# Kernel optimization log

Hardware: AMD Instinct MI355X
Metric: run time of the kernel (lower is better)

Reference implementation:

```python
import jax, jax.numpy as jnp
import numpy as np

N = 100_000      # nodes
E = 1_600_000    # directed edges (avg degree 16)
F_IN = 128       # num_node_features
H = 8            # heads in conv1
C = 32           # hidden_channels
G = 64           # graphs in batch
NC = 10          # num_classes


def setup_inputs() -> dict:
    key = jax.random.key(0)
    ks = jax.random.split(key, 12)
    gl = lambda k, shape, fan: (jax.random.normal(k, shape, jnp.float32) / np.sqrt(fan)).astype(jnp.float32)
    return {
        "x": jax.random.normal(ks[0], (N, F_IN), jnp.float32),
        "edge_index": jax.random.randint(ks[1], (2, E), 0, N, dtype=jnp.int32),
        "batch": jnp.sort(jax.random.randint(ks[2], (N,), 0, G, dtype=jnp.int32)),
        "W1": gl(ks[3], (F_IN, H * C), F_IN),
        "att_src1": gl(ks[4], (H, C), C),
        "att_dst1": gl(ks[5], (H, C), C),
        "b1": jnp.zeros((H * C,), jnp.float32),
        "W2": gl(ks[6], (H * C, C), H * C),
        "att_src2": gl(ks[7], (1, C), C),
        "att_dst2": gl(ks[8], (1, C), C),
        "b2": jnp.zeros((C,), jnp.float32),
        "Wlin": gl(ks[9], (C, NC), C),
        "blin": jnp.zeros((NC,), jnp.float32),
    }


def gat_conv(x, src, dst, W, att_src, att_dst, bias, heads, ch, concat):
    """PyG GATConv (eval mode): gather, LeakyReLU(0.2) scores, segment softmax over dst, scatter-sum."""
    n = x.shape[0]
    h = (x @ W).reshape(n, heads, ch)                     # [N,H,C]
    a_s = jnp.sum(h * att_src, axis=-1)                   # [N,H]
    a_d = jnp.sum(h * att_dst, axis=-1)                   # [N,H]
    e = jax.nn.leaky_relu(a_s[src] + a_d[dst], 0.2)       # [E,H]
    m = jax.ops.segment_max(e, dst, num_segments=n)       # [N,H], stable softmax
    p = jnp.exp(e - m[dst])
    z = jax.ops.segment_sum(p, dst, num_segments=n)
    coef = p / (z[dst] + 1e-16)                           # [E,H]
    out = jax.ops.segment_sum(coef[:, :, None] * h[src], dst, num_segments=n)  # [N,H,C]
    out = out.reshape(n, heads * ch) if concat else out.mean(axis=1)
    return out + bias


def reference(x, edge_index, batch, W1, att_src1, att_dst1, b1,
              W2, att_src2, att_dst2, b2, Wlin, blin):
    n = x.shape[0]
    loops = jnp.arange(n, dtype=edge_index.dtype)         # GATConv add_self_loops=True
    src = jnp.concatenate([edge_index[0], loops])
    dst = jnp.concatenate([edge_index[1], loops])

    h = gat_conv(x, src, dst, W1, att_src1, att_dst1, b1, H, C, concat=True)
    h = jax.nn.elu(h)                                     # dropout is identity in eval
    h = gat_conv(h, src, dst, W2, att_src2, att_dst2, b2, 1, C, concat=False)

    # global_mean_pool over graph ids
    sums = jax.ops.segment_sum(h, batch, num_segments=G)  # [G,C]
    cnts = jax.ops.segment_sum(jnp.ones((n,), h.dtype), batch, num_segments=G)
    pooled = sums / jnp.maximum(cnts, 1.0)[:, None]

    return pooled @ Wlin + blin                           # [G,NC]
```

## Files before the change

### kernel.cpp

```cpp
#include <hip/hip_runtime.h>
#include <cstdint>

#define NN 100000
#define EE 1600000
#define GG 64
#define FIN 128
#define HC 256
#define NC 10

typedef short v8s __attribute__((ext_vector_type(8)));
typedef float v4f __attribute__((ext_vector_type(4)));

static __device__ __forceinline__ float lrelu(float x) { return x > 0.f ? x : 0.2f * x; }
static __device__ __forceinline__ float bf2f(unsigned short b) {
  return __uint_as_float(((unsigned int)b) << 16);
}
static __device__ __forceinline__ unsigned short f2bf(float f) {
  unsigned int u = __float_as_uint(f);
  unsigned int r = (u + 0x7FFFu + ((u >> 16) & 1u)) >> 16;
  return (unsigned short)r;
}
static __device__ __forceinline__ void unpack2(unsigned int u, float& f0, float& f1) {
  f0 = __uint_as_float(u << 16);
  f1 = __uint_as_float(u & 0xFFFF0000u);
}

__global__ __launch_bounds__(256) void k_prepx(const float* __restrict__ x,
                                               unsigned short* __restrict__ xb,
                                               const int* __restrict__ ei,
                                               int* __restrict__ counts) {
  const int idx = blockIdx.x * 256 + threadIdx.x;
  const int i4 = idx * 4;
  float4 v = *(const float4*)(x + i4);
  ushort4 u;
  u.x = f2bf(v.x); u.y = f2bf(v.y); u.z = f2bf(v.z); u.w = f2bf(v.w);
  *(ushort4*)(xb + i4) = u;
  if (idx < EE) atomicAdd(&counts[ei[EE + idx]], 1);
}

__global__ void k_prep(const float* __restrict__ W1, unsigned short* __restrict__ W1tg) {
  const int b = blockIdx.x, t = threadIdx.x;
  if (t < 128) W1tg[b * 128 + t] = f2bf(W1[t * HC + b]);
}

__global__ void k_prepw2(const float* __restrict__ W2,
                         unsigned short* __restrict__ W2thi,
                         unsigned short* __restrict__ W2tlo) {
  const int b = blockIdx.x;
  const int t = threadIdx.x;
  float w = W2[t * 32 + b];
  unsigned short hi = f2bf(w);
  W2thi[b * 256 + t] = hi;
  W2tlo[b * 256 + t] = f2bf(w - bf2f(hi));
}

__global__ __launch_bounds__(256) void k_gemm1(const unsigned short* __restrict__ xb,
                                               const unsigned short* __restrict__ W1tg,
                                               const float* __restrict__ att_src1,
                                               const float* __restrict__ att_dst1,
                                               unsigned short* __restrict__ h1b,
                                               float* __restrict__ as1,
                                               float* __restrict__ ad1) {
  const int t = threadIdx.x;
  const int m0 = blockIdx.x * 64;
  const int n0 = blockIdx.y * 128;
  const int hb = blockIdx.y * 4;
  const int lane = t & 63;
  const int wm = t >> 6;
  const int ml = lane & 15;
  const int quad = lane >> 4;
  int row = m0 + wm * 16 + ml; if (row >= NN) row = NN - 1;
  v4f acc[8];
#pragma unroll
  for (int tt = 0; tt < 8; ++tt) acc[tt] = (v4f){0.f, 0.f, 0.f, 0.f};
#pragma unroll
  for (int kk = 0; kk < 4; ++kk) {
    const int k0 = kk * 32 + quad * 8;
    v8s a = *(const v8s*)(xb + (size_t)row * FIN + k0);
#pragma unroll
    for (int tt = 0; tt < 8; ++tt) {
      v8s b = *(const v8s*)(W1tg + (size_t)(n0 + tt * 16 + ml) * FIN + k0);
      acc[tt] = __builtin_amdgcn_mfma_f32_16x16x32_bf16(a, b, acc[tt], 0, 0, 0);
    }
  }
#pragma unroll
  for (int tt = 0; tt < 8; ++tt) {
#pragma unroll
    for (int r = 0; r < 4; ++r) {
      int rg = m0 + wm * 16 + quad * 4 + r;
      if (rg < NN) h1b[(size_t)rg * HC + n0 + tt * 16 + ml] = f2bf(acc[tt][r]);
    }
  }
  float ps[4][4], pd[4][4];
#pragma unroll
  for (int i = 0; i < 4; ++i)
#pragma unroll
    for (int r = 0; r < 4; ++r) { ps[i][r] = 0.f; pd[i][r] = 0.f; }
#pragma unroll
  for (int i = 0; i < 4; ++i) {
#pragma unroll
    for (int half = 0; half < 2; ++half) {
      const int tt = 2 * i + half;
      const float a_s = att_src1[(hb + i) * 32 + half * 16 + ml];
      const float a_d = att_dst1[(hb + i) * 32 + half * 16 + ml];
#pragma unroll
      for (int r = 0; r < 4; ++r) {
        ps[i][r] += acc[tt][r] * a_s;
        pd[i][r] += acc[tt][r] * a_d;
      }
    }
  }
#pragma unroll
  for (int i = 0; i < 4; ++i) {
#pragma unroll
    for (int r = 0; r < 4; ++r) {
      float s = ps[i][r], d = pd[i][r];
      s += __shfl_xor(s, 1, 64); s += __shfl_xor(s, 2, 64);
      s += __shfl_xor(s, 4, 64); s += __shfl_xor(s, 8, 64);
      d += __shfl_xor(d, 1, 64); d += __shfl_xor(d, 2, 64);
      d += __shfl_xor(d, 4, 64); d += __shfl_xor(d, 8, 64);
      ps[i][r] = s; pd[i][r] = d;
    }
  }
  if (ml == 0) {
#pragma unroll
    for (int r = 0; r < 4; ++r) {
      int rg = m0 + wm * 16 + quad * 4 + r;
      if (rg < NN) {
#pragma unroll
        for (int i = 0; i < 4; ++i) {
          as1[rg * 8 + hb + i] = ps[i][r];
          ad1[rg * 8 + hb + i] = pd[i][r];
        }
      }
    }
  }
}

__global__ void k_scan1(const int* __restrict__ counts, int* __restrict__ offs,
                        int* __restrict__ bsums) {
  __shared__ int s[256];
  const int t = threadIdx.x;
  const int i = blockIdx.x * 256 + t;
  int v = (i < NN) ? counts[i] : 0;
  s[t] = v;
  __syncthreads();
  for (int off = 1; off < 256; off <<= 1) {
    int tv = (t >= off) ? s[t - off] : 0;
    __syncthreads();
    s[t] += tv;
    __syncthreads();
  }
  if (i < NN) offs[i] = s[t] - v;
  if (t == 255) bsums[blockIdx.x] = s[255];
}

__global__ void k_scan2(int* __restrict__ bsums, int nb) {
  __shared__ int s[512];
  const int t = threadIdx.x;
  int v = (t < nb) ? bsums[t] : 0;
  s[t] = v;
  __syncthreads();
  for (int off = 1; off < 512; off <<= 1) {
    int tv = (t >= off) ? s[t - off] : 0;
    __syncthreads();
    s[t] += tv;
    __syncthreads();
  }
  if (t < nb) bsums[t] = s[t] - v;
}

__global__ void k_scan3(int* __restrict__ offs, const int* __restrict__ bsums,
                        int* __restrict__ cursor) {
  const int i = blockIdx.x * 256 + threadIdx.x;
  if (i < NN) {
    int v = offs[i] + bsums[i >> 8];
    offs[i] = v;
    cursor[i] = v;
  }
  if (i == 0) offs[NN] = EE;
}

__global__ void k_scatter(const int* __restrict__ ei, int* __restrict__ cursor,
                          int* __restrict__ esrc) {
  int e = blockIdx.x * 256 + threadIdx.x;
  if (e < EE) {
    int s = ei[e];
    int d = ei[EE + e];
    int p = atomicAdd(&cursor[d], 1);
    esrc[p] = s;
  }
}

__global__ __launch_bounds__(256) void k_agg1(const unsigned short* __restrict__ h1b,
                                              const float* __restrict__ as1,
                                              const float* __restrict__ ad1,
                                              const int* __restrict__ offs,
                                              const int* __restrict__ esrc,
                                              const float* __restrict__ b1,
                                              const unsigned short* __restrict__ W2thi,
                                              const unsigned short* __restrict__ W2tlo,
                                              const float* __restrict__ att_src2,
                                              const float* __restrict__ att_dst2,
                                              unsigned short* __restrict__ h2b,
                                              float* __restrict__ as2,
                                              float* __restrict__ ad2) {
  __shared__ float wl[4][8][36];
  __shared__ __attribute__((aligned(16))) unsigned short o1hi[4][272];
  __shared__ __attribute__((aligned(16))) unsigned short o1lo[4][272];
  const int t = threadIdx.x;
  const int lane = t & 63;
  const int w = t >> 6;
  const int n0 = blockIdx.x * 4;
  const int nu = __builtin_amdgcn_readfirstlane(n0 + w);
  const int head = lane >> 3;
  const uint2* __restrict__ h1u2 = (const uint2*)h1b;
  const int start = offs[nu], end = offs[nu + 1];
  const float4 dnA = *(const float4*)(ad1 + (size_t)nu * 8);
  const float4 dnB = *(const float4*)(ad1 + (size_t)nu * 8 + 4);
  const float4 dn4 = (lane & 32) ? dnB : dnA;

  float z, a0, a1, a2, a3;
  {
    float w0 = __expf(lrelu(as1[nu * 8 + head] + ad1[nu * 8 + head]));
    uint2 q = h1u2[(size_t)nu * 64 + lane];
    float f0, f1, f2, f3; unpack2(q.x, f0, f1); unpack2(q.y, f2, f3);
    z = w0; a0 = w0 * f0; a1 = w0 * f1; a2 = w0 * f2; a3 = w0 * f3;
  }
  for (int base = start; base < end; base += 32) {
    const int cnt = min(32, end - base);
    const int l5 = lane & 31;
    int s = 0;
    if (l5 < cnt) s = esrc[base + l5];
    const int hb4 = (lane >> 5) << 2;
    const float4 av = *(const float4*)(as1 + (size_t)s * 8 + hb4);
    float w0 = __expf(lrelu(av.x + dn4.x));
    float w1 = __expf(lrelu(av.y + dn4.y));
    float w2 = __expf(lrelu(av.z + dn4.z));
    float w3 = __expf(lrelu(av.w + dn4.w));
    const bool act = l5 < cnt;
    wl[w][hb4 + 0][l5] = act ? w0 : 0.f;
    wl[w][hb4 + 1][l5] = act ? w1 : 0.f;
    wl[w][hb4 + 2][l5] = act ? w2 : 0.f;
    wl[w][hb4 + 3][l5] = act ? w3 : 0.f;
    const int cnt4 = (cnt + 3) & ~3;
    int jb = 0;
    for (; jb + 8 <= cnt4; jb += 8) {
      uint2 q[8];
#pragma unroll
      for (int u = 0; u < 8; ++u) {
        const int sj = esrc[base + jb + u];
        q[u] = h1u2[(size_t)sj * 64 + lane];
      }
      const float4 wq0 = *(const float4*)&wl[w][head][jb];
      const float4 wq1 = *(const float4*)&wl[w][head][jb + 4];
      z += ((wq0.x + wq0.y) + (wq0.z + wq0.w)) + ((wq1.x + wq1.y) + (wq1.z + wq1.w));
      float f0, f1, f2, f3;
      unpack2(q[0].x, f0, f1); unpack2(q[0].y, f2, f3);
      a0 += wq0.x * f0; a1 += wq0.x * f1; a2 += wq0.x * f2; a3 += wq0.x * f3;
      unpack2(q[1].x, f0, f1); unpack2(q[1].y, f2, f3);
      a0 += wq0.y * f0; a1 += wq0.y * f1; a2 += wq0.y * f2; a3 += wq0.y * f3;
      unpack2(q[2].x, f0, f1); unpack2(q[2].y, f2, f3);
      a0 += wq0.z * f0; a1 += wq0.z * f1; a2 += wq0.z * f2; a3 += wq0.z * f3;
      unpack2(q[3].x, f0, f1); unpack2(q[3].y, f2, f3);
      a0 += wq0.w * f0; a1 += wq0.w * f1; a2 += wq0.w * f2; a3 += wq0.w * f3;
      unpack2(q[4].x, f0, f1); unpack2(q[4].y, f2, f3);
      a0 += wq1.x * f0; a1 += wq1.x * f1; a2 += wq1.x * f2; a3 += wq1.x * f3;
      unpack2(q[5].x, f0, f1); unpack2(q[5].y, f2, f3);
      a0 += wq1.y * f0; a1 += wq1.y * f1; a2 += wq1.y * f2; a3 += wq1.y * f3;
      unpack2(q[6].x, f0, f1); unpack2(q[6].y, f2, f3);
      a0 += wq1.z * f0; a1 += wq1.z * f1; a2 += wq1.z * f2; a3 += wq1.z * f3;
      unpack2(q[7].x, f0, f1); unpack2(q[7].y, f2, f3);
      a0 += wq1.w * f0; a1 += wq1.w * f1; a2 += wq1.w * f2; a3 += wq1.w * f3;
    }
    if (jb < cnt4) {
      uint2 q[4];
#pragma unroll
      for (int u = 0; u < 4; ++u) {
        const int sj = esrc[base + jb + u];
        q[u] = h1u2[(size_t)sj * 64 + lane];
      }
      const float4 wq0 = *(const float4*)&wl[w][head][jb];
      z += (wq0.x + wq0.y) + (wq0.z + wq0.w);
      float f0, f1, f2, f3;
      unpack2(q[0].x, f0, f1); unpack2(q[0].y, f2, f3);
      a0 += wq0.x * f0; a1 += wq0.x * f1; a2 += wq0.x * f2; a3 += wq0.x * f3;
      unpack2(q[1].x, f0, f1); unpack2(q[1].y, f2, f3);
      a0 += wq0.y * f0; a1 += wq0.y * f1; a2 += wq0.y * f2; a3 += wq0.y * f3;
      unpack2(q[2].x, f0, f1); unpack2(q[2].y, f2, f3);
      a0 += wq0.z * f0; a1 += wq0.z * f1; a2 += wq0.z * f2; a3 += wq0.z * f3;
      unpack2(q[3].x, f0, f1); unpack2(q[3].y, f2, f3);
      a0 += wq0.w * f0; a1 += wq0.w * f1; a2 += wq0.w * f2; a3 += wq0.w * f3;
    }
  }
  {
    const float zi = 1.0f / (z + 1e-16f);
    const float4 bb = *(const float4*)(b1 + 4 * lane);
    float v0 = a0 * zi + bb.x;
    float v1 = a1 * zi + bb.y;
    float v2 = a2 * zi + bb.z;
    float v3 = a3 * zi + bb.w;
    v0 = v0 > 0.f ? v0 : (__expf(v0) - 1.0f);
    v1 = v1 > 0.f ? v1 : (__expf(v1) - 1.0f);
    v2 = v2 > 0.f ? v2 : (__expf(v2) - 1.0f);
    v3 = v3 > 0.f ? v3 : (__expf(v3) - 1.0f);
    ushort4 hh, ll;
    hh.x = f2bf(v0); hh.y = f2bf(v1); hh.z = f2bf(v2); hh.w = f2bf(v3);
    ll.x = f2bf(v0 - bf2f(hh.x));
    ll.y = f2bf(v1 - bf2f(hh.y));
    ll.z = f2bf(v2 - bf2f(hh.z));
    ll.w = f2bf(v3 - bf2f(hh.w));
    *(ushort4*)&o1hi[w][4 * lane] = hh;
    *(ushort4*)&o1lo[w][4 * lane] = ll;
  }
  __syncthreads();
  if (w == 0) {
    const int ml = lane & 15;
    const int quad = lane >> 4;
    const int mr = ml & 3;
    v4f acc[2];
    acc[0] = (v4f){0.f, 0.f, 0.f, 0.f};
    acc[1] = (v4f){0.f, 0.f, 0.f, 0.f};
#pragma unroll
    for (int kk = 0; kk < 8; ++kk) {
      const int k0 = kk * 32 + quad * 8;
      v8s ah = *(const v8s*)&o1hi[mr][k0];
      v8s al = *(const v8s*)&o1lo[mr][k0];
#pragma unroll
      for (int tt = 0; tt < 2; ++tt) {
        v8s bh = *(const v8s*)(W2thi + (size_t)(tt * 16 + ml) * 256 + k0);
        v8s bl = *(const v8s*)(W2tlo + (size_t)(tt * 16 + ml) * 256 + k0);
        acc[tt] = __builtin_amdgcn_mfma_f32_16x16x32_bf16(ah, bh, acc[tt], 0, 0, 0);
        acc[tt] = __builtin_amdgcn_mfma_f32_16x16x32_bf16(al, bh, acc[tt], 0, 0, 0);
        acc[tt] = __builtin_amdgcn_mfma_f32_16x16x32_bf16(ah, bl, acc[tt], 0, 0, 0);
      }
    }
    if (quad == 0) {
      const float s0 = att_src2[ml], s1 = att_src2[16 + ml];
      const float d0 = att_dst2[ml], d1 = att_dst2[16 + ml];
#pragma unroll
      for (int r = 0; r < 4; ++r) {
        const int nn = n0 + r;
        const float h0 = acc[0][r], h1v = acc[1][r];
        h2b[(size_t)nn * 32 + ml] = f2bf(h0);
        h2b[(size_t)nn * 32 + 16 + ml] = f2bf(h1v);
        float ps = h0 * s0 + h1v * s1;
        float pd = h0 * d0 + h1v * d1;
        ps += __shfl_xor(ps, 1, 64); ps += __shfl_xor(ps, 2, 64);
        ps += __shfl_xor(ps, 4, 64); ps += __shfl_xor(ps, 8, 64);
        pd += __shfl_xor(pd, 1, 64); pd += __shfl_xor(pd, 2, 64);
        pd += __shfl_xor(pd, 4, 64); pd += __shfl_xor(pd, 8, 64);
        if (ml == 0) { as2[nn] = ps; ad2[nn] = pd; }
      }
    }
  }
}

__global__ __launch_bounds__(256) void k_agg2(const unsigned short* __restrict__ h2b,
                                              const float* __restrict__ as2,
                                              const float* __restrict__ ad2,
                                              const int* __restrict__ offs,
                                              const int* __restrict__ esrc,
                                              const float* __restrict__ b2,
                                              float* __restrict__ h3) {
  __shared__ int2 swl[4][64];
  const int t = threadIdx.x;
  const int lane = t & 63;
  const int wv = t >> 6;
  const int n = __builtin_amdgcn_readfirstlane(blockIdx.x * 4 + wv);
  const int col = lane & 15;
  const int slot = lane >> 4;
  const unsigned int* __restrict__ h2u = (const unsigned int*)h2b;
  const int start = offs[n], end = offs[n + 1];
  const float adn = ad2[n];
  float z = 0.f, acc0 = 0.f, acc1 = 0.f;
  if (slot == 0) {
    float w0 = __expf(lrelu(as2[n] + adn));
    unsigned int q = h2u[(unsigned)(n * 16 + col)];
    float f0, f1; unpack2(q, f0, f1);
    z = w0; acc0 = w0 * f0; acc1 = w0 * f1;
  }
  for (int base = start; base < end; base += 64) {
    const int cnt = min(64, end - base);
    int s = 0; float wgt = 0.f;
    if (lane < cnt) {
      s = esrc[base + lane];
      wgt = __expf(lrelu(as2[s] + adn));
    }
    swl[wv][lane] = make_int2(s, __float_as_int(wgt));
    const int nit = (cnt + 7) >> 3;
#pragma unroll 2
    for (int j = 0; j < nit; ++j) {
      const int2 p0 = swl[wv][8 * j + slot];
      const int2 p1 = swl[wv][8 * j + 4 + slot];
      const unsigned int q0 = h2u[(unsigned)(p0.x * 16 + col)];
      const unsigned int q1 = h2u[(unsigned)(p1.x * 16 + col)];
      const float wj0 = __int_as_float(p0.y);
      const float wj1 = __int_as_float(p1.y);
      float f0, f1, g0, g1;
      unpack2(q0, f0, f1); unpack2(q1, g0, g1);
      z += wj0 + wj1;
      acc0 += wj0 * f0; acc0 += wj1 * g0;
      acc1 += wj0 * f1; acc1 += wj1 * g1;
    }
  }
  acc0 += __shfl_xor(acc0, 16, 64); acc0 += __shfl_xor(acc0, 32, 64);
  acc1 += __shfl_xor(acc1, 16, 64); acc1 += __shfl_xor(acc1, 32, 64);
  z    += __shfl_xor(z, 16, 64);    z    += __shfl_xor(z, 32, 64);
  if (slot == 0) {
    const float zi = 1.0f / (z + 1e-16f);
    float2 bb = *(const float2*)(b2 + 2 * col);
    float2 o;
    o.x = acc0 * zi + bb.x;
    o.y = acc1 * zi + bb.y;
    *(float2*)(h3 + (size_t)n * 32 + 2 * col) = o;
  }
}

__global__ __launch_bounds__(256) void k_poolfin(const float* __restrict__ h3,
                                                 const int* __restrict__ batch,
                                                 const float* __restrict__ Wlin,
                                                 const float* __restrict__ blin,
                                                 float* __restrict__ out) {
  __shared__ int bounds[2];
  __shared__ float red[8][33];
  __shared__ float mean[32];
  const int g = blockIdx.x;
  const int t = threadIdx.x;
  if (t < 2) {
    int target = g + t;
    int lo = 0, hi = NN;
    while (lo < hi) { int mid = (lo + hi) >> 1; if (batch[mid] < target) lo = mid + 1; else hi = mid; }
    bounds[t] = lo;
  }
  __syncthreads();
  const int lo = bounds[0], hi = bounds[1];
  const int rr = t >> 5, c = t & 31;
  float a = 0.f;
  for (int r = lo + rr; r < hi; r += 8) a += h3[(size_t)r * 32 + c];
  red[rr][c] = a;
  __syncthreads();
  if (rr == 0) {
    float s = 0.f;
#pragma unroll
    for (int i = 0; i < 8; ++i) s += red[i][c];
    float ct = (float)(hi - lo);
    ct = ct > 1.f ? ct : 1.f;
    mean[c] = s / ct;
  }
  __syncthreads();
  if (t < NC) {
    float acc = 0.f;
#pragma unroll
    for (int cc = 0; cc < 32; ++cc) acc += mean[cc] * Wlin[cc * NC + t];
    out[g * NC + t] = acc + blin[t];
  }
}

extern "C" void kernel_launch(void* const* d_in, const int* in_sizes, int n_in,
                              void* d_out, int out_size, void* d_ws, size_t ws_size,
                              hipStream_t stream) {
  const float* x        = (const float*)d_in[0];
  const int*   ei       = (const int*)d_in[1];
  const int*   batch    = (const int*)d_in[2];
  const float* W1       = (const float*)d_in[3];
  const float* att_src1 = (const float*)d_in[4];
  const float* att_dst1 = (const float*)d_in[5];
  const float* b1       = (const float*)d_in[6];
  const float* W2       = (const float*)d_in[7];
  const float* att_src2 = (const float*)d_in[8];
  const float* att_dst2 = (const float*)d_in[9];
  const float* b2       = (const float*)d_in[10];
  const float* Wlin     = (const float*)d_in[11];
  const float* blin     = (const float*)d_in[12];
  float* out = (float*)d_out;
  char* ws = (char*)d_ws;

  unsigned short* h1b   = (unsigned short*)(ws + 0);
  unsigned short* xb    = (unsigned short*)(ws + 51200000);
  float* h3     = (float*)(ws + 51200000);
  float* as1    = (float*)(ws + 76800000);
  float* ad1    = (float*)(ws + 80000000);
  int* counts   = (int*)(ws + 83200000);
  int* offs     = (int*)(ws + 83600000);
  int* cursor   = (int*)(ws + 84000256);
  int* esrc     = (int*)(ws + 84400256);
  int* bsums    = (int*)(ws + 90800320);
  unsigned short* h2b   = (unsigned short*)(ws + 90801920);
  float* as2    = (float*)(ws + 97201920);
  float* ad2    = (float*)(ws + 97601920);
  unsigned short* W1tg  = (unsigned short*)(ws + 98001920);
  unsigned short* W2thi = (unsigned short*)(ws + 98067456);
  unsigned short* W2tlo = (unsigned short*)(ws + 98083840);

  const int nb_scan = (NN + 255) / 256;

  hipMemsetAsync(counts, 0, NN * sizeof(int), stream);
  hipMemsetAsync(ws + 90800256, 0, 64, stream);
  k_prepx<<<12500, 256, 0, stream>>>(x, xb, ei, counts);
  k_prep<<<256, 128, 0, stream>>>(W1, W1tg);
  k_prepw2<<<32, 256, 0, stream>>>(W2, W2thi, W2tlo);

  dim3 g1((NN + 63) / 64, 2);
  k_gemm1<<<g1, 256, 0, stream>>>(xb, W1tg, att_src1, att_dst1, h1b, as1, ad1);

  k_scan1<<<nb_scan, 256, 0, stream>>>(counts, offs, bsums);
  k_scan2<<<1, 512, 0, stream>>>(bsums, nb_scan);
  k_scan3<<<nb_scan, 256, 0, stream>>>(offs, bsums, cursor);
  k_scatter<<<(EE + 255) / 256, 256, 0, stream>>>(ei, cursor, esrc);

  k_agg1<<<NN / 4, 256, 0, stream>>>(h1b, as1, ad1, offs, esrc, b1, W2thi, W2tlo,
                                     att_src2, att_dst2, h2b, as2, ad2);

  k_agg2<<<NN / 4, 256, 0, stream>>>(h2b, as2, ad2, offs, esrc, b2, h3);
  k_poolfin<<<GG, 256, 0, stream>>>(h3, batch, Wlin, blin, out);
}
```

Measured before the change: 622.4 us.

## Widen gathers in GAT aggregation kernels and merge prep kernels into one launch

The layer-1 aggregation now has each half-wave gather a full 512-byte h1 row with 16-byte loads, so two edges are processed in parallel per wave, and the halves are combined with a cross-half shuffle. Layer-2 aggregation likewise uses 8-byte loads with 8 edges per pass, reduced by a three-step shuffle. The three preprocessing kernels are merged into one launch to cut launch overhead. The aim is fewer, wider memory transactions per gathered row, at the cost of more registers per thread and extra shuffle reductions.

```diff
diff --git a/kernel.cpp b/kernel.cpp
--- a/kernel.cpp
+++ b/kernel.cpp
@@ -10,6 +10,7 @@
 
 typedef short v8s __attribute__((ext_vector_type(8)));
 typedef float v4f __attribute__((ext_vector_type(4)));
+typedef unsigned short u8s __attribute__((ext_vector_type(8)));
 
 static __device__ __forceinline__ float lrelu(float x) { return x > 0.f ? x : 0.2f * x; }
 static __device__ __forceinline__ float bf2f(unsigned short b) {
@@ -25,33 +26,35 @@
   f1 = __uint_as_float(u & 0xFFFF0000u);
 }
 
-__global__ __launch_bounds__(256) void k_prepx(const float* __restrict__ x,
-                                               unsigned short* __restrict__ xb,
-                                               const int* __restrict__ ei,
-                                               int* __restrict__ counts) {
-  const int idx = blockIdx.x * 256 + threadIdx.x;
-  const int i4 = idx * 4;
-  float4 v = *(const float4*)(x + i4);
-  ushort4 u;
-  u.x = f2bf(v.x); u.y = f2bf(v.y); u.z = f2bf(v.z); u.w = f2bf(v.w);
-  *(ushort4*)(xb + i4) = u;
-  if (idx < EE) atomicAdd(&counts[ei[EE + idx]], 1);
-}
-
-__global__ void k_prep(const float* __restrict__ W1, unsigned short* __restrict__ W1tg) {
-  const int b = blockIdx.x, t = threadIdx.x;
-  if (t < 128) W1tg[b * 128 + t] = f2bf(W1[t * HC + b]);
-}
-
-__global__ void k_prepw2(const float* __restrict__ W2,
-                         unsigned short* __restrict__ W2thi,
-                         unsigned short* __restrict__ W2tlo) {
+__global__ __launch_bounds__(256) void k_prepall(const float* __restrict__ x,
+                                                 unsigned short* __restrict__ xb,
+                                                 const int* __restrict__ ei,
+                                                 int* __restrict__ counts,
+                                                 const float* __restrict__ W1,
+                                                 unsigned short* __restrict__ W1tg,
+                                                 const float* __restrict__ W2,
+                                                 unsigned short* __restrict__ W2thi,
+                                                 unsigned short* __restrict__ W2tlo) {
   const int b = blockIdx.x;
   const int t = threadIdx.x;
-  float w = W2[t * 32 + b];
-  unsigned short hi = f2bf(w);
-  W2thi[b * 256 + t] = hi;
-  W2tlo[b * 256 + t] = f2bf(w - bf2f(hi));
+  if (b < 12500) {
+    const int idx = b * 256 + t;
+    const int i4 = idx * 4;
+    float4 v = *(const float4*)(x + i4);
+    ushort4 u;
+    u.x = f2bf(v.x); u.y = f2bf(v.y); u.z = f2bf(v.z); u.w = f2bf(v.w);
+    *(ushort4*)(xb + i4) = u;
+    if (idx < EE) atomicAdd(&counts[ei[EE + idx]], 1);
+  } else if (b < 12756) {
+    const int n = b - 12500;
+    if (t < 128) W1tg[n * 128 + t] = f2bf(W1[t * HC + n]);
+  } else {
+    const int oc = b - 12756;
+    float wv = W2[t * 32 + oc];
+    unsigned short hi = f2bf(wv);
+    W2thi[oc * 256 + t] = hi;
+    W2tlo[oc * 256 + t] = f2bf(wv - bf2f(hi));
+  }
 }
 
 __global__ __launch_bounds__(256) void k_gemm1(const unsigned short* __restrict__ xb,
@@ -213,105 +216,121 @@
   const int w = t >> 6;
   const int n0 = blockIdx.x * 4;
   const int nu = __builtin_amdgcn_readfirstlane(n0 + w);
-  const int head = lane >> 3;
-  const uint2* __restrict__ h1u2 = (const uint2*)h1b;
+  const int hl = lane & 31;
+  const int half = lane >> 5;
+  const int head = hl >> 2;
+  const uint4* __restrict__ h1u4 = (const uint4*)h1b;
   const int start = offs[nu], end = offs[nu + 1];
   const float4 dnA = *(const float4*)(ad1 + (size_t)nu * 8);
   const float4 dnB = *(const float4*)(ad1 + (size_t)nu * 8 + 4);
   const float4 dn4 = (lane & 32) ? dnB : dnA;
 
-  float z, a0, a1, a2, a3;
+  float z, a0, a1, a2, a3, a4, a5, a6, a7;
   {
     float w0 = __expf(lrelu(as1[nu * 8 + head] + ad1[nu * 8 + head]));
-    uint2 q = h1u2[(size_t)nu * 64 + lane];
-    float f0, f1, f2, f3; unpack2(q.x, f0, f1); unpack2(q.y, f2, f3);
-    z = w0; a0 = w0 * f0; a1 = w0 * f1; a2 = w0 * f2; a3 = w0 * f3;
+    if (half) w0 = 0.f;
+    uint4 q = h1u4[(size_t)nu * 32 + hl];
+    float f0, f1, f2, f3, f4, f5, f6, f7;
+    unpack2(q.x, f0, f1); unpack2(q.y, f2, f3);
+    unpack2(q.z, f4, f5); unpack2(q.w, f6, f7);
+    z = w0;
+    a0 = w0 * f0; a1 = w0 * f1; a2 = w0 * f2; a3 = w0 * f3;
+    a4 = w0 * f4; a5 = w0 * f5; a6 = w0 * f6; a7 = w0 * f7;
   }
   for (int base = start; base < end; base += 32) {
     const int cnt = min(32, end - base);
-    const int l5 = lane & 31;
     int s = 0;
-    if (l5 < cnt) s = esrc[base + l5];
-    const int hb4 = (lane >> 5) << 2;
+    if (hl < cnt) s = esrc[base + hl];
+    const int hb4 = half << 2;
     const float4 av = *(const float4*)(as1 + (size_t)s * 8 + hb4);
     float w0 = __expf(lrelu(av.x + dn4.x));
     float w1 = __expf(lrelu(av.y + dn4.y));
     float w2 = __expf(lrelu(av.z + dn4.z));
     float w3 = __expf(lrelu(av.w + dn4.w));
-    const bool act = l5 < cnt;
-    wl[w][hb4 + 0][l5] = act ? w0 : 0.f;
-    wl[w][hb4 + 1][l5] = act ? w1 : 0.f;
-    wl[w][hb4 + 2][l5] = act ? w2 : 0.f;
-    wl[w][hb4 + 3][l5] = act ? w3 : 0.f;
+    const bool act = hl < cnt;
+    wl[w][hb4 + 0][hl] = act ? w0 : 0.f;
+    wl[w][hb4 + 1][hl] = act ? w1 : 0.f;
+    wl[w][hb4 + 2][hl] = act ? w2 : 0.f;
+    wl[w][hb4 + 3][hl] = act ? w3 : 0.f;
     const int cnt4 = (cnt + 3) & ~3;
     int jb = 0;
-    for (; jb + 8 <= cnt4; jb += 8) {
-      uint2 q[8];
+    for (; jb + 16 <= cnt4; jb += 16) {
+      uint4 q[8];
 #pragma unroll
       for (int u = 0; u < 8; ++u) {
-        const int sj = esrc[base + jb + u];
-        q[u] = h1u2[(size_t)sj * 64 + lane];
-      }
-      const float4 wq0 = *(const float4*)&wl[w][head][jb];
-      const float4 wq1 = *(const float4*)&wl[w][head][jb + 4];
-      z += ((wq0.x + wq0.y) + (wq0.z + wq0.w)) + ((wq1.x + wq1.y) + (wq1.z + wq1.w));
-      float f0, f1, f2, f3;
-      unpack2(q[0].x, f0, f1); unpack2(q[0].y, f2, f3);
-      a0 += wq0.x * f0; a1 += wq0.x * f1; a2 += wq0.x * f2; a3 += wq0.x * f3;
-      unpack2(q[1].x, f0, f1); unpack2(q[1].y, f2, f3);
-      a0 += wq0.y * f0; a1 += wq0.y * f1; a2 += wq0.y * f2; a3 += wq0.y * f3;
-      unpack2(q[2].x, f0, f1); unpack2(q[2].y, f2, f3);
-      a0 += wq0.z * f0; a1 += wq0.z * f1; a2 += wq0.z * f2; a3 += wq0.z * f3;
-      unpack2(q[3].x, f0, f1); unpack2(q[3].y, f2, f3);
-      a0 += wq0.w * f0; a1 += wq0.w * f1; a2 += wq0.w * f2; a3 += wq0.w * f3;
-      unpack2(q[4].x, f0, f1); unpack2(q[4].y, f2, f3);
-      a0 += wq1.x * f0; a1 += wq1.x * f1; a2 += wq1.x * f2; a3 += wq1.x * f3;
-      unpack2(q[5].x, f0, f1); unpack2(q[5].y, f2, f3);
-      a0 += wq1.y * f0; a1 += wq1.y * f1; a2 += wq1.y * f2; a3 += wq1.y * f3;
-      unpack2(q[6].x, f0, f1); unpack2(q[6].y, f2, f3);
-      a0 += wq1.z * f0; a1 += wq1.z * f1; a2 += wq1.z * f2; a3 += wq1.z * f3;
-      unpack2(q[7].x, f0, f1); unpack2(q[7].y, f2, f3);
-      a0 += wq1.w * f0; a1 += wq1.w * f1; a2 += wq1.w * f2; a3 += wq1.w * f3;
-    }
-    if (jb < cnt4) {
-      uint2 q[4];
-#pragma unroll
-      for (int u = 0; u < 4; ++u) {
-        const int sj = esrc[base + jb + u];
-        q[u] = h1u2[(size_t)sj * 64 + lane];
-      }
-      const float4 wq0 = *(const float4*)&wl[w][head][jb];
-      z += (wq0.x + wq0.y) + (wq0.z + wq0.w);
-      float f0, f1, f2, f3;
-      unpack2(q[0].x, f0, f1); unpack2(q[0].y, f2, f3);
-      a0 += wq0.x * f0; a1 += wq0.x * f1; a2 += wq0.x * f2; a3 += wq0.x * f3;
-      unpack2(q[1].x, f0, f1); unpack2(q[1].y, f2, f3);
-      a0 += wq0.y * f0; a1 += wq0.y * f1; a2 += wq0.y * f2; a3 += wq0.y * f3;
-      unpack2(q[2].x, f0, f1); unpack2(q[2].y, f2, f3);
-      a0 += wq0.z * f0; a1 += wq0.z * f1; a2 += wq0.z * f2; a3 += wq0.z * f3;
-      unpack2(q[3].x, f0, f1); unpack2(q[3].y, f2, f3);
-      a0 += wq0.w * f0; a1 += wq0.w * f1; a2 += wq0.w * f2; a3 += wq0.w * f3;
-    }
-  }
-  {
+        const int s0 = esrc[base + jb + 2 * u];
+        const int s1 = esrc[base + jb + 2 * u + 1];
+        const int sj = half ? s1 : s0;
+        q[u] = h1u4[(size_t)sj * 32 + hl];
+      }
+#pragma unroll
+      for (int u = 0; u < 8; ++u) {
+        const float2 wp = *(const float2*)&wl[w][head][jb + 2 * u];
+        const float we = half ? wp.y : wp.x;
+        float f0, f1, f2, f3, f4, f5, f6, f7;
+        unpack2(q[u].x, f0, f1); unpack2(q[u].y, f2, f3);
+        unpack2(q[u].z, f4, f5); unpack2(q[u].w, f6, f7);
+        z += we;
+        a0 += we * f0; a1 += we * f1; a2 += we * f2; a3 += we * f3;
+        a4 += we * f4; a5 += we * f5; a6 += we * f6; a7 += we * f7;
+      }
+    }
+    for (; jb < cnt4; jb += 4) {
+      uint4 q[2];
+#pragma unroll
+      for (int u = 0; u < 2; ++u) {
+        const int s0 = esrc[base + jb + 2 * u];
+        const int s1 = esrc[base + jb + 2 * u + 1];
+        const int sj = half ? s1 : s0;
+        q[u] = h1u4[(size_t)sj * 32 + hl];
+      }
+#pragma unroll
+      for (int u = 0; u < 2; ++u) {
+        const float2 wp = *(const float2*)&wl[w][head][jb + 2 * u];
+        const float we = half ? wp.y : wp.x;
+        float f0, f1, f2, f3, f4, f5, f6, f7;
+        unpack2(q[u].x, f0, f1); unpack2(q[u].y, f2, f3);
+        unpack2(q[u].z, f4, f5); unpack2(q[u].w, f6, f7);
+        z += we;
+        a0 += we * f0; a1 += we * f1; a2 += we * f2; a3 += we * f3;
+        a4 += we * f4; a5 += we * f5; a6 += we * f6; a7 += we * f7;
+      }
+    }
+  }
+  a0 += __shfl_xor(a0, 32, 64); a1 += __shfl_xor(a1, 32, 64);
+  a2 += __shfl_xor(a2, 32, 64); a3 += __shfl_xor(a3, 32, 64);
+  a4 += __shfl_xor(a4, 32, 64); a5 += __shfl_xor(a5, 32, 64);
+  a6 += __shfl_xor(a6, 32, 64); a7 += __shfl_xor(a7, 32, 64);
+  z  += __shfl_xor(z, 32, 64);
+  if (lane < 32) {
     const float zi = 1.0f / (z + 1e-16f);
-    const float4 bb = *(const float4*)(b1 + 4 * lane);
-    float v0 = a0 * zi + bb.x;
-    float v1 = a1 * zi + bb.y;
-    float v2 = a2 * zi + bb.z;
-    float v3 = a3 * zi + bb.w;
+    const float4 bb0 = *(const float4*)(b1 + 8 * hl);
+    const float4 bb1 = *(const float4*)(b1 + 8 * hl + 4);
+    float v0 = a0 * zi + bb0.x;
+    float v1 = a1 * zi + bb0.y;
+    float v2 = a2 * zi + bb0.z;
+    float v3 = a3 * zi + bb0.w;
+    float v4 = a4 * zi + bb1.x;
+    float v5 = a5 * zi + bb1.y;
+    float v6 = a6 * zi + bb1.z;
+    float v7 = a7 * zi + bb1.w;
     v0 = v0 > 0.f ? v0 : (__expf(v0) - 1.0f);
     v1 = v1 > 0.f ? v1 : (__expf(v1) - 1.0f);
     v2 = v2 > 0.f ? v2 : (__expf(v2) - 1.0f);
     v3 = v3 > 0.f ? v3 : (__expf(v3) - 1.0f);
-    ushort4 hh, ll;
-    hh.x = f2bf(v0); hh.y = f2bf(v1); hh.z = f2bf(v2); hh.w = f2bf(v3);
-    ll.x = f2bf(v0 - bf2f(hh.x));
-    ll.y = f2bf(v1 - bf2f(hh.y));
-    ll.z = f2bf(v2 - bf2f(hh.z));
-    ll.w = f2bf(v3 - bf2f(hh.w));
-    *(ushort4*)&o1hi[w][4 * lane] = hh;
-    *(ushort4*)&o1lo[w][4 * lane] = ll;
+    v4 = v4 > 0.f ? v4 : (__expf(v4) - 1.0f);
+    v5 = v5 > 0.f ? v5 : (__expf(v5) - 1.0f);
+    v6 = v6 > 0.f ? v6 : (__expf(v6) - 1.0f);
+    v7 = v7 > 0.f ? v7 : (__expf(v7) - 1.0f);
+    u8s hh, ll;
+    hh[0] = f2bf(v0); hh[1] = f2bf(v1); hh[2] = f2bf(v2); hh[3] = f2bf(v3);
+    hh[4] = f2bf(v4); hh[5] = f2bf(v5); hh[6] = f2bf(v6); hh[7] = f2bf(v7);
+    ll[0] = f2bf(v0 - bf2f(hh[0])); ll[1] = f2bf(v1 - bf2f(hh[1]));
+    ll[2] = f2bf(v2 - bf2f(hh[2])); ll[3] = f2bf(v3 - bf2f(hh[3]));
+    ll[4] = f2bf(v4 - bf2f(hh[4])); ll[5] = f2bf(v5 - bf2f(hh[5]));
+    ll[6] = f2bf(v6 - bf2f(hh[6])); ll[7] = f2bf(v7 - bf2f(hh[7]));
+    *(u8s*)&o1hi[w][8 * hl] = hh;
+    *(u8s*)&o1lo[w][8 * hl] = ll;
   }
   __syncthreads();
   if (w == 0) {
@@ -368,17 +387,18 @@
   const int lane = t & 63;
   const int wv = t >> 6;
   const int n = __builtin_amdgcn_readfirstlane(blockIdx.x * 4 + wv);
-  const int col = lane & 15;
-  const int slot = lane >> 4;
-  const unsigned int* __restrict__ h2u = (const unsigned int*)h2b;
+  const int g = lane >> 3;
+  const int sl = lane & 7;
+  const uint2* __restrict__ h2u2 = (const uint2*)h2b;
   const int start = offs[n], end = offs[n + 1];
   const float adn = ad2[n];
-  float z = 0.f, acc0 = 0.f, acc1 = 0.f;
-  if (slot == 0) {
+  float z, c0, c1, c2, c3;
+  {
     float w0 = __expf(lrelu(as2[n] + adn));
-    unsigned int q = h2u[(unsigned)(n * 16 + col)];
-    float f0, f1; unpack2(q, f0, f1);
-    z = w0; acc0 = w0 * f0; acc1 = w0 * f1;
+    if (g != 0) w0 = 0.f;
+    uint2 q = h2u2[(size_t)n * 8 + sl];
+    float f0, f1, f2, f3; unpack2(q.x, f0, f1); unpack2(q.y, f2, f3);
+    z = w0; c0 = w0 * f0; c1 = w0 * f1; c2 = w0 * f2; c3 = w0 * f3;
   }
   for (int base = start; base < end; base += 64) {
     const int cnt = min(64, end - base);
@@ -388,32 +408,43 @@
       wgt = __expf(lrelu(as2[s] + adn));
     }
     swl[wv][lane] = make_int2(s, __float_as_int(wgt));
-    const int nit = (cnt + 7) >> 3;
+    const int nit = (cnt + 15) >> 4;
 #pragma unroll 2
     for (int j = 0; j < nit; ++j) {
-      const int2 p0 = swl[wv][8 * j + slot];
-      const int2 p1 = swl[wv][8 * j + 4 + slot];
-      const unsigned int q0 = h2u[(unsigned)(p0.x * 16 + col)];
-      const unsigned int q1 = h2u[(unsigned)(p1.x * 16 + col)];
+      const int2 p0 = swl[wv][16 * j + g];
+      const int2 p1 = swl[wv][16 * j + 8 + g];
+      const uint2 q0 = h2u2[(size_t)p0.x * 8 + sl];
+      const uint2 q1 = h2u2[(size_t)p1.x * 8 + sl];
       const float wj0 = __int_as_float(p0.y);
       const float wj1 = __int_as_float(p1.y);
-      float f0, f1, g0, g1;
-      unpack2(q0, f0, f1); unpack2(q1, g0, g1);
+      float f0, f1, f2, f3, g0, g1, g2, g3;
+      unpack2(q0.x, f0, f1); unpack2(q0.y, f2, f3);
+      unpack2(q1.x, g0, g1); unpack2(q1.y, g2, g3);
       z += wj0 + wj1;
-      acc0 += wj0 * f0; acc0 += wj1 * g0;
-      acc1 += wj0 * f1; acc1 += wj1 * g1;
-    }
-  }
-  acc0 += __shfl_xor(acc0, 16, 64); acc0 += __shfl_xor(acc0, 32, 64);
-  acc1 += __shfl_xor(acc1, 16, 64); acc1 += __shfl_xor(acc1, 32, 64);
-  z    += __shfl_xor(z, 16, 64);    z    += __shfl_xor(z, 32, 64);
-  if (slot == 0) {
+      c0 += wj0 * f0; c0 += wj1 * g0;
+      c1 += wj0 * f1; c1 += wj1 * g1;
+      c2 += wj0 * f2; c2 += wj1 * g2;
+      c3 += wj0 * f3; c3 += wj1 * g3;
+    }
+  }
+  c0 += __shfl_xor(c0, 8, 64);  c1 += __shfl_xor(c1, 8, 64);
+  c2 += __shfl_xor(c2, 8, 64);  c3 += __shfl_xor(c3, 8, 64);
+  z  += __shfl_xor(z, 8, 64);
+  c0 += __shfl_xor(c0, 16, 64); c1 += __shfl_xor(c1, 16, 64);
+  c2 += __shfl_xor(c2, 16, 64); c3 += __shfl_xor(c3, 16, 64);
+  z  += __shfl_xor(z, 16, 64);
+  c0 += __shfl_xor(c0, 32, 64); c1 += __shfl_xor(c1, 32, 64);
+  c2 += __shfl_xor(c2, 32, 64); c3 += __shfl_xor(c3, 32, 64);
+  z  += __shfl_xor(z, 32, 64);
+  if (lane < 8) {
     const float zi = 1.0f / (z + 1e-16f);
-    float2 bb = *(const float2*)(b2 + 2 * col);
-    float2 o;
-    o.x = acc0 * zi + bb.x;
-    o.y = acc1 * zi + bb.y;
-    *(float2*)(h3 + (size_t)n * 32 + 2 * col) = o;
+    const float4 bb = *(const float4*)(b2 + 4 * sl);
+    float4 o;
+    o.x = c0 * zi + bb.x;
+    o.y = c1 * zi + bb.y;
+    o.z = c2 * zi + bb.z;
+    o.w = c3 * zi + bb.w;
+    *(float4*)(h3 + (size_t)n * 32 + 4 * sl) = o;
   }
 }
 
@@ -497,9 +528,7 @@
 
   hipMemsetAsync(counts, 0, NN * sizeof(int), stream);
   hipMemsetAsync(ws + 90800256, 0, 64, stream);
-  k_prepx<<<12500, 256, 0, stream>>>(x, xb, ei, counts);
-  k_prep<<<256, 128, 0, stream>>>(W1, W1tg);
-  k_prepw2<<<32, 256, 0, stream>>>(W2, W2thi, W2tlo);
+  k_prepall<<<12788, 256, 0, stream>>>(x, xb, ei, counts, W1, W1tg, W2, W2thi, W2tlo);
 
   dim3 g1((NN + 63) / 64, 2);
   k_gemm1<<<g1, 256, 0, stream>>>(xb, W1tg, att_src1, att_dst1, h1b, as1, ad1);
```

Measured after the change: 627.4 us. About the same (+0.8%).
